# Kernel optimization log

Measured on AMD Instinct MI355X. Metric: run time of the kernel, lower is better.

## Reference

```python
import jax, jax.numpy as jnp
import numpy as np

NH = 10
EPS = 1e-10

def setup_inputs() -> dict:
    key = jax.random.key(0)
    k1, k2, k3, k4, k5 = jax.random.split(key, 5)
    b, n_s, e, n_t = 8, 8192, 32, 8192
    return {
        "x": jax.random.normal(k1, (b, n_s, e), dtype=jnp.float32),
        "rel_lon": jax.random.normal(k2, (n_t, n_s), dtype=jnp.float32),
        "rel_lat": jax.random.normal(k3, (n_t, n_s), dtype=jnp.float32),
        "coords_source": jax.random.uniform(k4, (n_s, 2), dtype=jnp.float32),
        "coords_target": jax.random.uniform(k5, (n_t, 2), dtype=jnp.float32),
    }

def reference(x, rel_lon, rel_lat, coords_source, coords_target):
    # ---- nn_layer: k-NN over precomputed relative coordinate matrices ----
    d_rel = jnp.sqrt(rel_lon ** 2 + rel_lat ** 2)          # [n_t, n_s]
    neg_d, idx = jax.lax.top_k(-d_rel, NH)                 # nh smallest distances
    indices_dist = -neg_d                                  # [n_t, nh]
    x_nearest = x[:, idx]                                  # [b, n_t, nh, e] gather
    indices_lon = jnp.take_along_axis(rel_lon, idx, axis=1)  # [n_t, nh]
    indices_lat = jnp.take_along_axis(rel_lat, idx, axis=1)  # [n_t, nh]
    # ---- interpolator: inverse-distance-weighted interpolation ----
    # pairwise target-source distances via the expanded form (avoids [n_t,n_s,2])
    t2 = jnp.sum(coords_target ** 2, axis=1)[:, None]      # [n_t, 1]
    s2 = jnp.sum(coords_source ** 2, axis=1)[None, :]      # [1, n_s]
    d2 = t2 + s2 - 2.0 * coords_target @ coords_source.T   # [n_t, n_s]
    d_ts = jnp.sqrt(jnp.maximum(d2, 1e-12))
    w = 1.0 / (d_ts + EPS)
    w = w / jnp.sum(w, axis=1, keepdims=True)              # [n_t, n_s]
    x_inter = jnp.einsum('bse,ts->bte', x, w)              # [b, n_t, e]
    return (x_nearest, x_inter, indices_dist, indices_lon, indices_lat)
```

## Files before the change

### kernel.cpp

```cpp
#include <hip/hip_runtime.h>
#include <hip/hip_bf16.h>
#include <stdint.h>

#define B_   8
#define NS_  8192
#define E_   32
#define NT_  8192
#define NH_  10
#define NCH_ 128
#define QCAP 128

typedef __bf16 bf16x8 __attribute__((ext_vector_type(8)));
typedef float  f32x4  __attribute__((ext_vector_type(4)));
typedef unsigned short ushort8_t __attribute__((ext_vector_type(8)));
typedef unsigned short ushort4_t __attribute__((ext_vector_type(4)));

static __device__ inline unsigned short f2bf(float f) {
  __hip_bfloat16 h = __float2bfloat16(f);
  return *reinterpret_cast<unsigned short*>(&h);
}
static __device__ inline float bf2f(unsigned short u) {
  __hip_bfloat16 h;
  *reinterpret_cast<unsigned short*>(&h) = u;
  return __bfloat162float(h);
}

static __device__ inline float tenth_smallest(float v, int lane) {
  unsigned long long kv =
      ((unsigned long long)__float_as_uint(v) << 32) | (unsigned)lane;
  float out = 0.f;
#pragma unroll
  for (int k = 0; k < NH_; ++k) {
    unsigned long long m = kv;
#pragma unroll
    for (int off = 32; off > 0; off >>= 1) {
      const unsigned long long o = __shfl_xor(m, off, 64);
      m = o < m ? o : m;
    }
    if (kv == m) kv = ~0ull;
    if (k == NH_ - 1) out = __uint_as_float((unsigned)(m >> 32));
  }
  return out;
}

__global__ __launch_bounds__(256, 8) void topk_kernel(
    const float* __restrict__ rel_lon, const float* __restrict__ rel_lat,
    float* __restrict__ out_d, float* __restrict__ out_lon,
    float* __restrict__ out_lat, int* __restrict__ idx_out)
{
  __shared__ int cnt[4];
  __shared__ unsigned int cand[4][QCAP];

  const int q = threadIdx.x >> 6;
  const int lane = threadIdx.x & 63;
  const int t = blockIdx.x;
  const float* lon_row = rel_lon + (size_t)t * NS_;
  const float* lat_row = rel_lat + (size_t)t * NS_;
  const int base = q * 2048;
  const float4* lon4 = (const float4*)(lon_row + base);
  const float4* lat4 = (const float4*)(lat_row + base);

  if (lane == 0) cnt[q] = 0;

  const float4 lo0 = lon4[0 * 64 + lane], la0 = lat4[0 * 64 + lane];
  const float4 lo1 = lon4[1 * 64 + lane], la1 = lat4[1 * 64 + lane];
  float d2a[4], d2b[4];
  d2a[0] = __fmaf_rn(lo0.x, lo0.x, __fmul_rn(la0.x, la0.x));
  d2a[1] = __fmaf_rn(lo0.y, lo0.y, __fmul_rn(la0.y, la0.y));
  d2a[2] = __fmaf_rn(lo0.z, lo0.z, __fmul_rn(la0.z, la0.z));
  d2a[3] = __fmaf_rn(lo0.w, lo0.w, __fmul_rn(la0.w, la0.w));
  d2b[0] = __fmaf_rn(lo1.x, lo1.x, __fmul_rn(la1.x, la1.x));
  d2b[1] = __fmaf_rn(lo1.y, lo1.y, __fmul_rn(la1.y, la1.y));
  d2b[2] = __fmaf_rn(lo1.z, lo1.z, __fmul_rn(la1.z, la1.z));
  d2b[3] = __fmaf_rn(lo1.w, lo1.w, __fmul_rn(la1.w, la1.w));
  const float lmin =
      fminf(fminf(fminf(d2a[0], d2a[1]), fminf(d2a[2], d2a[3])),
            fminf(fminf(d2b[0], d2b[1]), fminf(d2b[2], d2b[3])));
  const float T = tenth_smallest(lmin, lane) * 1.000002f;

#pragma unroll
  for (int j = 0; j < 4; ++j) {
    if (d2a[j] <= T) {
      const int pos = atomicAdd(&cnt[q], 1);
      if (pos < QCAP) cand[q][pos] = (unsigned)(base + lane * 4 + j);
    }
  }
#pragma unroll
  for (int j = 0; j < 4; ++j) {
    if (d2b[j] <= T) {
      const int pos = atomicAdd(&cnt[q], 1);
      if (pos < QCAP) cand[q][pos] = (unsigned)(base + 256 + lane * 4 + j);
    }
  }

#pragma unroll
  for (int p = 2; p < 8; ++p) {
    const float4 lo = lon4[p * 64 + lane];
    const float4 la = lat4[p * 64 + lane];
    float dv[4];
    dv[0] = __fmaf_rn(lo.x, lo.x, __fmul_rn(la.x, la.x));
    dv[1] = __fmaf_rn(lo.y, lo.y, __fmul_rn(la.y, la.y));
    dv[2] = __fmaf_rn(lo.z, lo.z, __fmul_rn(la.z, la.z));
    dv[3] = __fmaf_rn(lo.w, lo.w, __fmul_rn(la.w, la.w));
    const float mn = fminf(fminf(dv[0], dv[1]), fminf(dv[2], dv[3]));
    if (mn <= T) {
      const int s = base + p * 256 + lane * 4;
#pragma unroll
      for (int j = 0; j < 4; ++j) {
        if (dv[j] <= T) {
          const int pos = atomicAdd(&cnt[q], 1);
          if (pos < QCAP) cand[q][pos] = (unsigned)(s + j);
        }
      }
    }
  }

  __syncthreads();

  if (q == 0) {
    unsigned long long top[NH_];
#pragma unroll
    for (int i = 0; i < NH_; ++i) top[i] = ~0ull;

#pragma unroll
    for (int seg = 0; seg < 4; ++seg) {
      const int nc = min(cnt[seg], QCAP);
#pragma unroll
      for (int cc = 0; cc < QCAP / 64; ++cc) {
        const int ci = lane + cc * 64;
        if (ci < nc) {
          const unsigned s = cand[seg][ci];
          const float lo = lon_row[s];
          const float la = lat_row[s];
          const float d = __fsqrt_rn(__fadd_rn(__fmul_rn(lo, lo),
                                               __fmul_rn(la, la)));
          unsigned long long p =
              ((unsigned long long)__float_as_uint(d) << 32) | s;
#pragma unroll
          for (int i = 0; i < NH_; ++i) {
            const bool lt = p < top[i];
            const unsigned long long mn2 = lt ? p : top[i];
            const unsigned long long mx2 = lt ? top[i] : p;
            top[i] = mn2;
            p = mx2;
          }
        }
      }
    }

    unsigned long long resv = ~0ull;
    unsigned long long cur = top[0];
#pragma unroll
    for (int k = 0; k < NH_; ++k) {
      unsigned long long m = cur;
#pragma unroll
      for (int off = 32; off > 0; off >>= 1) {
        const unsigned long long o = __shfl_xor(m, off, 64);
        m = o < m ? o : m;
      }
      if (cur == m) {
#pragma unroll
        for (int i = 0; i < NH_ - 1; ++i) top[i] = top[i + 1];
        top[NH_ - 1] = ~0ull;
        cur = top[0];
      }
      if (lane == k) resv = m;
    }

    if (lane < NH_) {
      const unsigned s = (unsigned)(resv & 0xffffffffu);
      const float d = __uint_as_float((unsigned)(resv >> 32));
      out_d[t * NH_ + lane] = d;
      idx_out[t * NH_ + lane] = (int)s;
      out_lon[t * NH_ + lane] = lon_row[s];
      out_lat[t * NH_ + lane] = lat_row[s];
    }
  }
}

__global__ __launch_bounds__(256) void gather_kernel(
    const float* __restrict__ x, const int* __restrict__ idxbuf,
    float* __restrict__ out_xn)
{
  const int t = blockIdx.x;
  __shared__ int sidx[NH_];
  if (threadIdx.x < NH_) sidx[threadIdx.x] = idxbuf[t * NH_ + threadIdx.x];
  __syncthreads();
  for (int i = threadIdx.x; i < B_ * NH_ * (E_ / 4); i += 256) {
    const int e4 = i & 7;
    const int k = (i >> 3) % NH_;
    const int b = (i >> 3) / NH_;
    const int s = sidx[k];
    const float4 v = *(const float4*)(x + ((size_t)b * NS_ + s) * E_ + e4 * 4);
    *(float4*)(out_xn + (((size_t)b * NT_ + t) * NH_ + k) * E_ + e4 * 4) = v;
  }
}

__global__ __launch_bounds__(256) void xprep_kernel(
    const float* __restrict__ x, unsigned short* __restrict__ XT2)
{
  __shared__ __align__(16) unsigned short T[32][136];
  const int b = blockIdx.y;
  const int s0 = blockIdx.x * 128;
  const int tid = threadIdx.x;
  const int eq = tid & 7, slq = tid >> 3;
#pragma unroll
  for (int r4 = 0; r4 < 4; ++r4) {
    const int sl = r4 * 32 + slq;
    const float4 v = *(const float4*)&x[((size_t)b * NS_ + s0 + sl) * E_ + eq * 4];
    T[eq * 4 + 0][sl] = f2bf(v.x);
    T[eq * 4 + 1][sl] = f2bf(v.y);
    T[eq * 4 + 2][sl] = f2bf(v.z);
    T[eq * 4 + 3][sl] = f2bf(v.w);
  }
  __syncthreads();
  const int r = tid & 31, cq = tid >> 5;
  const int be = b * 32 + r;
  const int sA = s0 + cq * 16;
  const int c = sA >> 6;
  const int kA = (sA >> 3) & 7;
  unsigned short* dst = XT2 + ((size_t)(c * 8 + kA) * 256 + be) * 8;
  *(ushort8_t*)dst = *(const ushort8_t*)&T[r][cq * 16];
  *(ushort8_t*)(dst + 2048) = *(const ushort8_t*)&T[r][cq * 16 + 8];
}

__global__ __launch_bounds__(512) void xinter_mfma(
    const unsigned short* __restrict__ XT2, const float* __restrict__ cs,
    const float* __restrict__ ct, float* __restrict__ out_xi)
{
#pragma clang fp contract(off)
  __shared__ __align__(16) unsigned short Xl[2][8][256][8];
  __shared__ __align__(16) unsigned short Rl[2][8][16][8];
  __shared__ float RsumP[16][32];
  __shared__ float RsumInv[32];

  const int tid = threadIdx.x;
  const int w = tid >> 6, l = tid & 63;
  const int mg = w >> 1, ng = w & 1;
  const int lcol = l & 15, lkg = l >> 4;
  const int t0 = blockIdx.x * 32;

  const int gt = tid & 31;
  const int gq = tid >> 5;
  const int gng = gt >> 4, glc = gt & 15;
  const int gk = gq >> 1;
  const int gsl = (gq & 1) * 4;
  const float2 ctg = ((const float2*)ct)[t0 + gt];
  const float t2g = ctg.x * ctg.x + ctg.y * ctg.y;
  float rpart = 0.f;

  const int t = t0 + ng * 16 + lcol;

  f32x4 acc[4];
#pragma unroll
  for (int m = 0; m < 4; ++m)
#pragma unroll
    for (int j = 0; j < 4; ++j) acc[m][j] = 0.f;

#define STAGE_CHUNK(buf, ch)                                                 \
  {                                                                          \
    const unsigned short* gsrc =                                             \
        XT2 + ((size_t)(ch) * 8 + w) * 2048 + (size_t)l * 8;                 \
    _Pragma("unroll")                                                        \
    for (int bg = 0; bg < 4; ++bg) {                                         \
      __builtin_amdgcn_global_load_lds(                                      \
          (const __attribute__((address_space(1))) void*)(gsrc + bg * 512),  \
          (__attribute__((address_space(3))) void*)&Xl[buf][w][bg * 64][0],  \
          16, 0, 0);                                                         \
    }                                                                        \
  }

  STAGE_CHUNK(0, 0);
  asm volatile("s_waitcnt vmcnt(0)" ::: "memory");
  __builtin_amdgcn_s_barrier();

  int cur = 0;
  for (int c = 0; c < NCH_; ++c) {
    if (c + 1 < NCH_) STAGE_CHUNK(cur ^ 1, c + 1);

    {
      const int sb = c * 64 + gq * 4;
      const float4 cA = *(const float4*)&cs[2 * sb];
      const float4 cB = *(const float4*)&cs[2 * sb + 4];
      const float sxv[4] = {cA.x, cA.z, cB.x, cB.z};
      const float syv[4] = {cA.y, cA.w, cB.y, cB.w};
      ushort4_t ro;
#pragma unroll
      for (int j = 0; j < 4; ++j) {
        const float sx = sxv[j], sy = syv[j];
        const float s2 = sx * sx + sy * sy;
        const float p0 = ctg.x * sx;
        const float dot = fmaf(ctg.y, sy, p0);
        const float ts = t2g + s2;
        float d2 = ts - 2.0f * dot;
        d2 = fmaxf(d2, 1e-12f);
        const float r = __builtin_amdgcn_rsqf(d2);
        const unsigned short ub = f2bf(r);
        ro[j] = ub;
        rpart += bf2f(ub);
      }
      *(ushort4_t*)&Rl[gng][gk][glc][gsl] = ro;
    }
    asm volatile("s_waitcnt lgkmcnt(0)" ::: "memory");
    __builtin_amdgcn_s_barrier();

#pragma unroll
    for (int half = 0; half < 2; ++half) {
      const bf16x8 Bf = *(const bf16x8*)&Rl[ng][half * 4 + lkg][lcol][0];
#pragma unroll
      for (int m = 0; m < 4; ++m) {
        const bf16x8 a =
            *(const bf16x8*)&Xl[cur][half * 4 + lkg][(mg * 4 + m) * 16 + lcol][0];
        acc[m] = __builtin_amdgcn_mfma_f32_16x16x32_bf16(a, Bf, acc[m], 0, 0, 0);
      }
    }

    asm volatile("s_waitcnt vmcnt(0)" ::: "memory");
    __builtin_amdgcn_s_barrier();
    cur ^= 1;
  }
#undef STAGE_CHUNK

  RsumP[gq][gt] = rpart;
  asm volatile("s_waitcnt lgkmcnt(0)" ::: "memory");
  __builtin_amdgcn_s_barrier();
  if (tid < 32) {
    float ssum = 0.f;
#pragma unroll
    for (int qq = 0; qq < 16; ++qq) ssum += RsumP[qq][tid];
    RsumInv[tid] = 1.0f / ssum;
  }
  asm volatile("s_waitcnt lgkmcnt(0)" ::: "memory");
  __builtin_amdgcn_s_barrier();
  const float ri = RsumInv[ng * 16 + lcol];

#pragma unroll
  for (int m = 0; m < 4; ++m) {
    const int be0 = (mg * 4 + m) * 16 + lkg * 4;
    const int b = be0 >> 5, e = be0 & 31;
    float4 o;
    o.x = acc[m][0] * ri;
    o.y = acc[m][1] * ri;
    o.z = acc[m][2] * ri;
    o.w = acc[m][3] * ri;
    *(float4*)&out_xi[((size_t)b * NT_ + t) * E_ + e] = o;
  }
}

extern "C" void kernel_launch(void* const* d_in, const int* in_sizes, int n_in,
                              void* d_out, int out_size, void* d_ws,
                              size_t ws_size, hipStream_t stream)
{
  const float* x       = (const float*)d_in[0];
  const float* rel_lon = (const float*)d_in[1];
  const float* rel_lat = (const float*)d_in[2];
  const float* cs      = (const float*)d_in[3];
  const float* ct      = (const float*)d_in[4];

  float* out = (float*)d_out;
  float* out_xn  = out;
  float* out_xi  = out + (size_t)B_ * NT_ * NH_ * E_;
  float* out_d   = out_xi + (size_t)B_ * NT_ * E_;
  float* out_lon = out_d + (size_t)NT_ * NH_;
  float* out_lat = out_lon + (size_t)NT_ * NH_;

  int* idxbuf = (int*)d_ws;
  unsigned short* XT2 = (unsigned short*)out_xn;

  topk_kernel<<<NT_, 256, 0, stream>>>(rel_lon, rel_lat, out_d, out_lon,
                                       out_lat, idxbuf);
  xprep_kernel<<<dim3(NS_ / 128, B_), 256, 0, stream>>>(x, XT2);
  xinter_mfma<<<NT_ / 32, 512, 0, stream>>>(XT2, cs, ct, out_xi);
  gather_kernel<<<NT_, 256, 0, stream>>>(x, idxbuf, out_xn);
}
```

Baseline: 289.2 us.

## Stage top-k distance rows through LDS with async global-to-LDS loads

The top-k kernel now issues all of a wave's lon/lat loads up front as direct global-to-LDS transfers. It then waits on them stage by stage with explicit vmcnt waits and computes squared distances from LDS. The candidate threshold is now taken from the minimum over all eight chunks instead of the first two, which tightens the filter and should reduce candidate atomics. In exchange, each block uses 64KB of shared memory and the occupancy hint is dropped, which limits how many blocks can be resident per CU for this bandwidth-bound pass.

```diff
diff --git a/kernel.cpp b/kernel.cpp
--- a/kernel.cpp
+++ b/kernel.cpp
@@ -25,6 +25,19 @@
   return __bfloat162float(h);
 }
 
+static __device__ inline void wait_vm(int n) {
+  switch (n) {
+    case 0:  asm volatile("s_waitcnt vmcnt(0)" ::: "memory"); break;
+    case 2:  asm volatile("s_waitcnt vmcnt(2)" ::: "memory"); break;
+    case 4:  asm volatile("s_waitcnt vmcnt(4)" ::: "memory"); break;
+    case 6:  asm volatile("s_waitcnt vmcnt(6)" ::: "memory"); break;
+    case 8:  asm volatile("s_waitcnt vmcnt(8)" ::: "memory"); break;
+    case 10: asm volatile("s_waitcnt vmcnt(10)" ::: "memory"); break;
+    case 12: asm volatile("s_waitcnt vmcnt(12)" ::: "memory"); break;
+    default: asm volatile("s_waitcnt vmcnt(14)" ::: "memory"); break;
+  }
+}
+
 static __device__ inline float tenth_smallest(float v, int lane) {
   unsigned long long kv =
       ((unsigned long long)__float_as_uint(v) << 32) | (unsigned)lane;
@@ -43,11 +56,13 @@
   return out;
 }
 
-__global__ __launch_bounds__(256, 8) void topk_kernel(
+__global__ __launch_bounds__(256) void topk_kernel(
     const float* __restrict__ rel_lon, const float* __restrict__ rel_lat,
     float* __restrict__ out_d, float* __restrict__ out_lon,
     float* __restrict__ out_lat, int* __restrict__ idx_out)
 {
+  __shared__ __align__(16) float LonB[4][2048];
+  __shared__ __align__(16) float LatB[4][2048];
   __shared__ int cnt[4];
   __shared__ unsigned int cand[4][QCAP];
 
@@ -57,57 +72,49 @@
   const float* lon_row = rel_lon + (size_t)t * NS_;
   const float* lat_row = rel_lat + (size_t)t * NS_;
   const int base = q * 2048;
-  const float4* lon4 = (const float4*)(lon_row + base);
-  const float4* lat4 = (const float4*)(lat_row + base);
+  const float* lonq = lon_row + base;
+  const float* latq = lat_row + base;
 
   if (lane == 0) cnt[q] = 0;
 
-  const float4 lo0 = lon4[0 * 64 + lane], la0 = lat4[0 * 64 + lane];
-  const float4 lo1 = lon4[1 * 64 + lane], la1 = lat4[1 * 64 + lane];
-  float d2a[4], d2b[4];
-  d2a[0] = __fmaf_rn(lo0.x, lo0.x, __fmul_rn(la0.x, la0.x));
-  d2a[1] = __fmaf_rn(lo0.y, lo0.y, __fmul_rn(la0.y, la0.y));
-  d2a[2] = __fmaf_rn(lo0.z, lo0.z, __fmul_rn(la0.z, la0.z));
-  d2a[3] = __fmaf_rn(lo0.w, lo0.w, __fmul_rn(la0.w, la0.w));
-  d2b[0] = __fmaf_rn(lo1.x, lo1.x, __fmul_rn(la1.x, la1.x));
-  d2b[1] = __fmaf_rn(lo1.y, lo1.y, __fmul_rn(la1.y, la1.y));
-  d2b[2] = __fmaf_rn(lo1.z, lo1.z, __fmul_rn(la1.z, la1.z));
-  d2b[3] = __fmaf_rn(lo1.w, lo1.w, __fmul_rn(la1.w, la1.w));
-  const float lmin =
-      fminf(fminf(fminf(d2a[0], d2a[1]), fminf(d2a[2], d2a[3])),
-            fminf(fminf(d2b[0], d2b[1]), fminf(d2b[2], d2b[3])));
+#pragma unroll
+  for (int p = 0; p < 8; ++p) {
+    __builtin_amdgcn_global_load_lds(
+        (const __attribute__((address_space(1))) void*)(lonq + p * 256 +
+                                                        lane * 4),
+        (__attribute__((address_space(3))) void*)&LonB[q][p * 256], 16, 0, 0);
+    __builtin_amdgcn_global_load_lds(
+        (const __attribute__((address_space(1))) void*)(latq + p * 256 +
+                                                        lane * 4),
+        (__attribute__((address_space(3))) void*)&LatB[q][p * 256], 16, 0, 0);
+  }
+
+  float d2v[8][4];
+  float lmin = __uint_as_float(0x7f800000u);
+#pragma unroll
+  for (int p = 0; p < 8; ++p) {
+    wait_vm(14 - 2 * p);
+    const float4 lo = *(const float4*)&LonB[q][p * 256 + lane * 4];
+    const float4 la = *(const float4*)&LatB[q][p * 256 + lane * 4];
+    d2v[p][0] = __fmaf_rn(lo.x, lo.x, __fmul_rn(la.x, la.x));
+    d2v[p][1] = __fmaf_rn(lo.y, lo.y, __fmul_rn(la.y, la.y));
+    d2v[p][2] = __fmaf_rn(lo.z, lo.z, __fmul_rn(la.z, la.z));
+    d2v[p][3] = __fmaf_rn(lo.w, lo.w, __fmul_rn(la.w, la.w));
+    lmin = fminf(lmin, fminf(fminf(d2v[p][0], d2v[p][1]),
+                             fminf(d2v[p][2], d2v[p][3])));
+  }
+
   const float T = tenth_smallest(lmin, lane) * 1.000002f;
 
 #pragma unroll
-  for (int j = 0; j < 4; ++j) {
-    if (d2a[j] <= T) {
-      const int pos = atomicAdd(&cnt[q], 1);
-      if (pos < QCAP) cand[q][pos] = (unsigned)(base + lane * 4 + j);
-    }
-  }
-#pragma unroll
-  for (int j = 0; j < 4; ++j) {
-    if (d2b[j] <= T) {
-      const int pos = atomicAdd(&cnt[q], 1);
-      if (pos < QCAP) cand[q][pos] = (unsigned)(base + 256 + lane * 4 + j);
-    }
-  }
-
-#pragma unroll
-  for (int p = 2; p < 8; ++p) {
-    const float4 lo = lon4[p * 64 + lane];
-    const float4 la = lat4[p * 64 + lane];
-    float dv[4];
-    dv[0] = __fmaf_rn(lo.x, lo.x, __fmul_rn(la.x, la.x));
-    dv[1] = __fmaf_rn(lo.y, lo.y, __fmul_rn(la.y, la.y));
-    dv[2] = __fmaf_rn(lo.z, lo.z, __fmul_rn(la.z, la.z));
-    dv[3] = __fmaf_rn(lo.w, lo.w, __fmul_rn(la.w, la.w));
-    const float mn = fminf(fminf(dv[0], dv[1]), fminf(dv[2], dv[3]));
+  for (int p = 0; p < 8; ++p) {
+    const float mn = fminf(fminf(d2v[p][0], d2v[p][1]),
+                           fminf(d2v[p][2], d2v[p][3]));
     if (mn <= T) {
       const int s = base + p * 256 + lane * 4;
 #pragma unroll
       for (int j = 0; j < 4; ++j) {
-        if (dv[j] <= T) {
+        if (d2v[p][j] <= T) {
           const int pos = atomicAdd(&cnt[q], 1);
           if (pos < QCAP) cand[q][pos] = (unsigned)(s + j);
         }
```

Measured after the change: 368.3 us. 1.27x slower.
